# Kernel tuning notes

Hardware: AMD Instinct MI355X
Metric: run time of the kernel (lower is better)

## Reference

```python
import jax, jax.numpy as jnp
import numpy as np

# Config matching init_kwargs
D_MODEL = 1024   # input_size
D_HEAD = 2048    # head_size (expert hidden)
N_EXPERTS = 8
TOP_K = 2


def setup_inputs() -> dict:
    key = jax.random.key(0)
    k_x, k_g, k_w1, k_b1, k_w2, k_b2 = jax.random.split(key, 6)
    B, S = 4, 1024
    x = jax.random.normal(k_x, (B, S, D_MODEL), dtype=jnp.float32)
    # f_gate: nn.Linear(input_size, num_experts, bias=False) -> weight [E, D]
    gate_w = jax.random.normal(k_g, (N_EXPERTS, D_MODEL), dtype=jnp.float32) * 0.02
    # experts: ParallelExperts weights [E, in, out]
    s1 = 1.0 / D_MODEL
    s2 = 1.0 / D_HEAD
    w1 = jax.random.uniform(k_w1, (N_EXPERTS, D_MODEL, D_HEAD), jnp.float32, -s1, s1)
    b1 = jax.random.uniform(k_b1, (N_EXPERTS, D_HEAD), jnp.float32, -s1, s1)
    w2 = jax.random.uniform(k_w2, (N_EXPERTS, D_HEAD, D_MODEL), jnp.float32, -s2, s2)
    b2 = jax.random.uniform(k_b2, (N_EXPERTS, D_MODEL), jnp.float32, -s2, s2)
    return {"x": x, "gate_w": gate_w, "w1": w1, "b1": b1, "w2": w2, "b2": b2}


def reference(x, gate_w, w1, b1, w2, b2):
    B, S, D = x.shape
    xt = x.reshape(-1, D)                                   # [N, D]
    N = xt.shape[0]
    # --- gating (noisy_gating=False, eval path of top_k_gating) ---
    logits = xt @ gate_w.T                                  # [N, E]
    probs = jax.nn.softmax(logits, axis=-1)
    top_g, top_i = jax.lax.top_k(probs, TOP_K)              # [N, k]
    # gates = zeros.scatter(1, top_k_indices, top_k_gates)
    gates = jnp.zeros_like(probs).at[jnp.arange(N)[:, None], top_i].set(top_g)  # [N, E]
    # --- dispatch / grouped GEMM / combine ---
    # Equivalent dense-per-expert form: gates[n,e]==0 for non-routed tokens,
    # so y[n] = sum_e gates[n,e] * f_e(x[n]) exactly matches the
    # sort/scatter + per-expert torch.mm dispatch of ParallelLinear.
    y = jnp.zeros_like(xt)
    for e in range(N_EXPERTS):
        h = jax.nn.gelu(xt @ w1[e] + b1[e], approximate=False)  # [N, H]
        y = y + gates[:, e:e + 1] * (h @ w2[e] + b2[e])
    return y.reshape(B, S, D)
```

## Files before the change

### kernel.cpp

```cpp
#include <hip/hip_runtime.h>
#include <hip/hip_bf16.h>
#include <cstdint>
#include <cstddef>

#define N_TOK 4096
#define DM    1024
#define DH    2048
#define NE    8
#define BM    128
#define BN    128
#define BK    64
#define MAXT  80
#define HROWS (MAXT * BM)

typedef unsigned short u16t;
typedef __attribute__((ext_vector_type(4))) float          f32x4;
typedef __attribute__((ext_vector_type(8))) unsigned short u16x8;

__device__ __forceinline__ u16t f2b(float f) {
  union { float f; unsigned u; } v; v.f = f;
  return (u16t)((v.u + 0x7FFFu + ((v.u >> 16) & 1u)) >> 16);
}

__device__ __forceinline__ void gload16(const void* g, void* l) {
  auto gp = (const __attribute__((address_space(1))) unsigned int*)(uintptr_t)g;
  auto lp = (__attribute__((address_space(3))) unsigned int*)(uintptr_t)l;
  __builtin_amdgcn_global_load_lds(gp, lp, 16, 0, 0);
}

__device__ __forceinline__ void mfma16(f32x4& c, u16x8 a, u16x8 b) {
  asm("v_mfma_f32_16x16x32_bf16 %0, %1, %2, %0" : "+v"(c) : "v"(a), "v"(b));
}

__global__ void k_cvt_x(const float* __restrict__ x, u16t* __restrict__ x16) {
  int i = blockIdx.x * blockDim.x + threadIdx.x;
  float4 v = reinterpret_cast<const float4*>(x)[i];
  ushort4 o;
  o.x = f2b(v.x); o.y = f2b(v.y); o.z = f2b(v.z); o.w = f2b(v.w);
  reinterpret_cast<ushort4*>(x16)[i] = o;
}

__global__ void k_tr_cvt(const float* __restrict__ src, u16t* __restrict__ dst, int R, int C) {
  __shared__ float t[64][65];
  const float* s = src + (size_t)blockIdx.z * R * C;
  u16t* d = dst + (size_t)blockIdx.z * R * C;
  int r0 = blockIdx.y * 64, c0 = blockIdx.x * 64;
#pragma unroll
  for (int i = 0; i < 16; ++i) {
    int idx = i * 256 + threadIdx.x;
    int r = idx >> 6, c = idx & 63;
    t[r][c] = s[(size_t)(r0 + r) * C + (c0 + c)];
  }
  __syncthreads();
#pragma unroll
  for (int i = 0; i < 16; ++i) {
    int idx = i * 256 + threadIdx.x;
    int rr = idx >> 6, cc = idx & 63;
    d[(size_t)(c0 + rr) * R + (r0 + cc)] = f2b(t[cc][rr]);
  }
}

__global__ void __launch_bounds__(256) k_gate(const float* __restrict__ x,
                                              const float* __restrict__ gw,
                                              int* __restrict__ topi,
                                              float* __restrict__ topg) {
  __shared__ float gws[NE * DM];
  int tid = threadIdx.x;
#pragma unroll
  for (int i = 0; i < NE * DM / 256; ++i) gws[i * 256 + tid] = gw[i * 256 + tid];
  __syncthreads();
  int wv = tid >> 6, lane = tid & 63;
  int t = blockIdx.x * 4 + wv;
  float acc[NE];
#pragma unroll
  for (int e = 0; e < NE; ++e) acc[e] = 0.f;
  const float* xr = x + (size_t)t * DM;
#pragma unroll
  for (int c = 0; c < DM / 64; ++c) {
    float xv = xr[c * 64 + lane];
#pragma unroll
    for (int e = 0; e < NE; ++e) acc[e] += xv * gws[e * DM + c * 64 + lane];
  }
#pragma unroll
  for (int e = 0; e < NE; ++e) {
#pragma unroll
    for (int m = 1; m < 64; m <<= 1) acc[e] += __shfl_xor(acc[e], m);
  }
  float mx = acc[0];
#pragma unroll
  for (int e = 1; e < NE; ++e) mx = fmaxf(mx, acc[e]);
  float p[NE], s = 0.f;
#pragma unroll
  for (int e = 0; e < NE; ++e) { p[e] = expf(acc[e] - mx); s += p[e]; }
  float inv = 1.f / s;
#pragma unroll
  for (int e = 0; e < NE; ++e) p[e] *= inv;
  int i1 = 0; float g1 = p[0];
#pragma unroll
  for (int e = 1; e < NE; ++e) if (p[e] > g1) { g1 = p[e]; i1 = e; }
  int i2 = -1; float g2 = -1.f;
#pragma unroll
  for (int e = 0; e < NE; ++e) if (e != i1 && p[e] > g2) { g2 = p[e]; i2 = e; }
  if (lane == 0) {
    topi[t * 2 + 0] = i1; topi[t * 2 + 1] = i2;
    topg[t * 2 + 0] = g1; topg[t * 2 + 1] = g2;
  }
}

__global__ void __launch_bounds__(1024) k_scan(const int* __restrict__ topi,
                                               int* __restrict__ offe,
                                               int* __restrict__ cur64,
                                               int* __restrict__ te,
                                               int* __restrict__ trs,
                                               int* __restrict__ tnr,
                                               int* __restrict__ ntiles) {
  __shared__ int hist[NE];
  int tid = threadIdx.x;
  if (tid < NE) { hist[tid] = 0; cur64[tid * 16] = 0; }
  __syncthreads();
  int lc[NE];
#pragma unroll
  for (int e = 0; e < NE; ++e) lc[e] = 0;
#pragma unroll
  for (int i = 0; i < (N_TOK * 2) / 1024; ++i) {
    int v = topi[tid * ((N_TOK * 2) / 1024) + i];
#pragma unroll
    for (int e = 0; e < NE; ++e) lc[e] += (v == e);
  }
#pragma unroll
  for (int e = 0; e < NE; ++e) {
#pragma unroll
    for (int m = 1; m < 64; m <<= 1) lc[e] += __shfl_xor(lc[e], m);
  }
  if ((tid & 63) == 0) {
#pragma unroll
    for (int e = 0; e < NE; ++e) atomicAdd(&hist[e], lc[e]);
  }
  __syncthreads();
  if (tid == 0) {
    int off = 0, nt = 0;
    for (int e = 0; e < NE; ++e) {
      offe[e] = off;
      int c = hist[e];
      for (int i = 0; i < c; i += BM) {
        te[nt] = e; trs[nt] = off + i; tnr[nt] = min(BM, c - i); ++nt;
      }
      off += c;
    }
    *ntiles = nt;
  }
}

__global__ void k_scatter(const int* __restrict__ topi, const int* __restrict__ offe,
                          int* __restrict__ cur64, int* __restrict__ pair) {
  int t = blockIdx.x * blockDim.x + threadIdx.x;
  int lane = threadIdx.x & 63;
#pragma unroll
  for (int s = 0; s < 2; ++s) {
    int e = topi[t * 2 + s];
    int pos = 0;
#pragma unroll
    for (int ee = 0; ee < NE; ++ee) {
      unsigned long long mask = __ballot(e == ee);
      if (e == ee) {
        int rank = __popcll(mask & ((1ull << lane) - 1ull));
        int leader = __ffsll((long long)mask) - 1;
        int base = 0;
        if (lane == leader) base = atomicAdd(&cur64[ee * 16], (int)__popcll(mask));
        base = __shfl(base, leader);
        pos = offe[ee] + base + rank;
      }
    }
    pair[pos] = t * 2 + s;
  }
}

__global__ void __launch_bounds__(256, 2) k_gemm1(
    const u16t* __restrict__ x16, const u16t* __restrict__ w1t,
    const float* __restrict__ b1, u16t* __restrict__ h16,
    const int* __restrict__ pair, const int* __restrict__ te,
    const int* __restrict__ trs, const int* __restrict__ tnr,
    const int* __restrict__ ntiles) {
  int ty = blockIdx.y;
  if (ty >= *ntiles) return;
  int e = te[ty], rs = trs[ty], nr = tnr[ty];
  int n0 = blockIdx.x * BN;
  __shared__ u16t As[BM * BK];
  __shared__ u16t Bs[BN * BK];
  __shared__ int tok[BM];
  int tid = threadIdx.x;
  if (tid < BM) {
    int r = tid;
    int p = rs + (r < nr ? r : nr - 1);
    tok[r] = pair[p] >> 1;
  }
  __syncthreads();
  const u16t* aptr[4]; const u16t* bptr[4];
#pragma unroll
  for (int it = 0; it < 4; ++it) {
    int idx = it * 256 + tid;
    int r = idx >> 3, c = idx & 7;
    int cs = c ^ (r & 7);
    aptr[it] = x16 + (size_t)tok[r] * DM + cs * 8;
    bptr[it] = w1t + (size_t)e * DH * DM + (size_t)(n0 + r) * DM + cs * 8;
  }
  f32x4 acc[4][4];
#pragma unroll
  for (int m = 0; m < 4; ++m)
#pragma unroll
    for (int n = 0; n < 4; ++n) acc[m][n] = {0.f, 0.f, 0.f, 0.f};
  int lane = tid & 63, wv = tid >> 6;
  int wr = (wv >> 1) * 64, wc = (wv & 1) * 64;
  for (int k0 = 0; k0 < DM; k0 += BK) {
#pragma unroll
    for (int it = 0; it < 4; ++it) {
      int idx = it * 256 + tid;
      gload16(aptr[it] + k0, &As[idx * 8]);
      gload16(bptr[it] + k0, &Bs[idx * 8]);
    }
    __syncthreads();
#pragma unroll
    for (int kk = 0; kk < 2; ++kk) {
      u16x8 af[4], bf[4];
#pragma unroll
      for (int m = 0; m < 4; ++m) {
        int row = wr + m * 16 + (lane & 15);
        int cs = (kk * 4 + (lane >> 4)) ^ (row & 7);
        af[m] = *reinterpret_cast<const u16x8*>(&As[row * BK + cs * 8]);
      }
#pragma unroll
      for (int n = 0; n < 4; ++n) {
        int row = wc + n * 16 + (lane & 15);
        int cs = (kk * 4 + (lane >> 4)) ^ (row & 7);
        bf[n] = *reinterpret_cast<const u16x8*>(&Bs[row * BK + cs * 8]);
      }
#pragma unroll
      for (int m = 0; m < 4; ++m)
#pragma unroll
        for (int n = 0; n < 4; ++n) mfma16(acc[m][n], af[m], bf[n]);
    }
    __syncthreads();
  }
#pragma unroll
  for (int n = 0; n < 4; ++n) {
    int col = n0 + wc + n * 16 + (lane & 15);
    float bias = b1[e * DH + col];
#pragma unroll
    for (int m = 0; m < 4; ++m) {
#pragma unroll
      for (int r = 0; r < 4; ++r) {
        int rl = wr + m * 16 + ((lane >> 4) << 2) + r;
        if (rl < nr) {
          float z = acc[m][n][r] + bias;
          float g = 0.5f * z * (1.0f + erff(z * 0.70710678118654752440f));
          h16[(size_t)(rs + rl) * DH + col] = f2b(g);
        }
      }
    }
  }
}

__global__ void __launch_bounds__(256, 2) k_gemm2(
    const u16t* __restrict__ h16, const u16t* __restrict__ w2t,
    const float* __restrict__ b2, float* __restrict__ out,
    const int* __restrict__ pair, const float* __restrict__ topg,
    const int* __restrict__ te, const int* __restrict__ trs,
    const int* __restrict__ tnr, const int* __restrict__ ntiles) {
  int ty = blockIdx.y;
  if (ty >= *ntiles) return;
  int e = te[ty], rs = trs[ty], nr = tnr[ty];
  int n0 = blockIdx.x * BN;
  __shared__ u16t As[BM * BK];
  __shared__ u16t Bs[BN * BK];
  __shared__ int tsl[BM];
  __shared__ float gl[BM];
  int tid = threadIdx.x;
  if (tid < BM) {
    int r = tid;
    int p = rs + (r < nr ? r : nr - 1);
    int ts = pair[p];
    tsl[r] = ts;
    gl[r] = topg[ts];
  }
  __syncthreads();
  const u16t* aptr[4]; const u16t* bptr[4];
#pragma unroll
  for (int it = 0; it < 4; ++it) {
    int idx = it * 256 + tid;
    int r = idx >> 3, c = idx & 7;
    int cs = c ^ (r & 7);
    aptr[it] = h16 + (size_t)(rs + r) * DH + cs * 8;
    bptr[it] = w2t + (size_t)e * DM * DH + (size_t)(n0 + r) * DH + cs * 8;
  }
  f32x4 acc[4][4];
#pragma unroll
  for (int m = 0; m < 4; ++m)
#pragma unroll
    for (int n = 0; n < 4; ++n) acc[m][n] = {0.f, 0.f, 0.f, 0.f};
  int lane = tid & 63, wv = tid >> 6;
  int wr = (wv >> 1) * 64, wc = (wv & 1) * 64;
  for (int k0 = 0; k0 < DH; k0 += BK) {
#pragma unroll
    for (int it = 0; it < 4; ++it) {
      int idx = it * 256 + tid;
      gload16(aptr[it] + k0, &As[idx * 8]);
      gload16(bptr[it] + k0, &Bs[idx * 8]);
    }
    __syncthreads();
#pragma unroll
    for (int kk = 0; kk < 2; ++kk) {
      u16x8 af[4], bf[4];
#pragma unroll
      for (int m = 0; m < 4; ++m) {
        int row = wr + m * 16 + (lane & 15);
        int cs = (kk * 4 + (lane >> 4)) ^ (row & 7);
        af[m] = *reinterpret_cast<const u16x8*>(&As[row * BK + cs * 8]);
      }
#pragma unroll
      for (int n = 0; n < 4; ++n) {
        int row = wc + n * 16 + (lane & 15);
        int cs = (kk * 4 + (lane >> 4)) ^ (row & 7);
        bf[n] = *reinterpret_cast<const u16x8*>(&Bs[row * BK + cs * 8]);
      }
#pragma unroll
      for (int m = 0; m < 4; ++m)
#pragma unroll
        for (int n = 0; n < 4; ++n) mfma16(acc[m][n], af[m], bf[n]);
    }
    __syncthreads();
  }
  float bias[4];
#pragma unroll
  for (int n = 0; n < 4; ++n) bias[n] = b2[e * DM + n0 + wc + n * 16 + (lane & 15)];
#pragma unroll
  for (int m = 0; m < 4; ++m) {
#pragma unroll
    for (int r = 0; r < 4; ++r) {
      int rl = wr + m * 16 + ((lane >> 4) << 2) + r;
      if (rl < nr) {
        int ts = tsl[rl];
        float g = gl[rl];
        float* orow = out + (size_t)(ts >> 1) * DM;
#pragma unroll
        for (int n = 0; n < 4; ++n) {
          int col = n0 + wc + n * 16 + (lane & 15);
          float v = g * (acc[m][n][r] + bias[n]);
          unsafeAtomicAdd(&orow[col], v);
        }
      }
    }
  }
}

extern "C" void kernel_launch(void* const* d_in, const int* in_sizes, int n_in,
                              void* d_out, int out_size, void* d_ws, size_t ws_size,
                              hipStream_t stream) {
  const float* x  = (const float*)d_in[0];
  const float* gw = (const float*)d_in[1];
  const float* w1 = (const float*)d_in[2];
  const float* b1 = (const float*)d_in[3];
  const float* w2 = (const float*)d_in[4];
  const float* b2 = (const float*)d_in[5];
  float* out = (float*)d_out;
  char* ws = (char*)d_ws;

  size_t o = 0;
  auto alloc = [&](size_t b) { size_t p = o; o += (b + 255) & ~(size_t)255; return p; };
  size_t X16  = alloc((size_t)N_TOK * DM * 2);
  size_t W1T  = alloc((size_t)NE * DH * DM * 2);
  size_t W2T  = alloc((size_t)NE * DM * DH * 2);
  size_t HB   = alloc((size_t)HROWS * DH * 2);
  size_t TOPI = alloc((size_t)N_TOK * 2 * 4);
  size_t TOPG = alloc((size_t)N_TOK * 2 * 4);
  size_t PAIR = alloc((size_t)HROWS * 4);
  size_t CUR  = alloc(NE * 64);
  size_t OFE  = alloc(64);
  size_t TE   = alloc(MAXT * 4);
  size_t TRS  = alloc(MAXT * 4);
  size_t TNR  = alloc(MAXT * 4);
  size_t NT   = alloc(64);
  (void)ws_size; (void)in_sizes; (void)n_in;

  hipMemsetAsync(out, 0, (size_t)out_size * 4, stream);

  k_cvt_x<<<N_TOK * DM / 1024, 256, 0, stream>>>(x, (u16t*)(ws + X16));
  k_tr_cvt<<<dim3(DH / 64, DM / 64, NE), 256, 0, stream>>>(w1, (u16t*)(ws + W1T), DM, DH);
  k_tr_cvt<<<dim3(DM / 64, DH / 64, NE), 256, 0, stream>>>(w2, (u16t*)(ws + W2T), DH, DM);
  k_gate<<<N_TOK / 4, 256, 0, stream>>>(x, gw, (int*)(ws + TOPI), (float*)(ws + TOPG));
  k_scan<<<1, 1024, 0, stream>>>((int*)(ws + TOPI), (int*)(ws + OFE), (int*)(ws + CUR),
                                 (int*)(ws + TE), (int*)(ws + TRS), (int*)(ws + TNR),
                                 (int*)(ws + NT));
  k_scatter<<<N_TOK / 256, 256, 0, stream>>>((int*)(ws + TOPI), (int*)(ws + OFE),
                                             (int*)(ws + CUR), (int*)(ws + PAIR));
  k_gemm1<<<dim3(DH / BN, MAXT), 256, 0, stream>>>(
      (const u16t*)(ws + X16), (const u16t*)(ws + W1T), b1, (u16t*)(ws + HB),
      (const int*)(ws + PAIR), (const int*)(ws + TE), (const int*)(ws + TRS),
      (const int*)(ws + TNR), (const int*)(ws + NT));
  k_gemm2<<<dim3(DM / BN, MAXT), 256, 0, stream>>>(
      (const u16t*)(ws + HB), (const u16t*)(ws + W2T), b2, out,
      (const int*)(ws + PAIR), (const float*)(ws + TOPG), (const int*)(ws + TE),
      (const int*)(ws + TRS), (const int*)(ws + TNR), (const int*)(ws + NT));
}
```

Before: 221.0 us.

## Double-buffer LDS tiles in both expert GEMM kernels to overlap loads

Both grouped GEMM kernels now use two LDS buffers for the A and B tiles. The next K-slice is prefetched into the alternate buffer while MFMAs consume the current one, which hides global-load latency behind compute. The cost is double the LDS per block (about 64KB plus metadata), which may limit the two-blocks-per-CU occupancy target. The trailing synchronisation presumably still separates iterations.

```diff
diff --git a/kernel.cpp b/kernel.cpp
--- a/kernel.cpp
+++ b/kernel.cpp
@@ -185,8 +185,8 @@
   if (ty >= *ntiles) return;
   int e = te[ty], rs = trs[ty], nr = tnr[ty];
   int n0 = blockIdx.x * BN;
-  __shared__ u16t As[BM * BK];
-  __shared__ u16t Bs[BN * BK];
+  __shared__ u16t As[2][BM * BK];
+  __shared__ u16t Bs[2][BN * BK];
   __shared__ int tok[BM];
   int tid = threadIdx.x;
   if (tid < BM) {
@@ -211,14 +211,25 @@
     for (int n = 0; n < 4; ++n) acc[m][n] = {0.f, 0.f, 0.f, 0.f};
   int lane = tid & 63, wv = tid >> 6;
   int wr = (wv >> 1) * 64, wc = (wv & 1) * 64;
-  for (int k0 = 0; k0 < DM; k0 += BK) {
-#pragma unroll
-    for (int it = 0; it < 4; ++it) {
-      int idx = it * 256 + tid;
-      gload16(aptr[it] + k0, &As[idx * 8]);
-      gload16(bptr[it] + k0, &Bs[idx * 8]);
-    }
-    __syncthreads();
+#pragma unroll
+  for (int it = 0; it < 4; ++it) {
+    int idx = it * 256 + tid;
+    gload16(aptr[it], &As[0][idx * 8]);
+    gload16(bptr[it], &Bs[0][idx * 8]);
+  }
+  __syncthreads();
+  const int NK = DM / BK;
+  for (int ks = 0; ks < NK; ++ks) {
+    int cur = ks & 1;
+    if (ks + 1 < NK) {
+      int k1 = (ks + 1) * BK;
+#pragma unroll
+      for (int it = 0; it < 4; ++it) {
+        int idx = it * 256 + tid;
+        gload16(aptr[it] + k1, &As[cur ^ 1][idx * 8]);
+        gload16(bptr[it] + k1, &Bs[cur ^ 1][idx * 8]);
+      }
+    }
 #pragma unroll
     for (int kk = 0; kk < 2; ++kk) {
       u16x8 af[4], bf[4];
@@ -226,13 +237,13 @@
       for (int m = 0; m < 4; ++m) {
         int row = wr + m * 16 + (lane & 15);
         int cs = (kk * 4 + (lane >> 4)) ^ (row & 7);
-        af[m] = *reinterpret_cast<const u16x8*>(&As[row * BK + cs * 8]);
+        af[m] = *reinterpret_cast<const u16x8*>(&As[cur][row * BK + cs * 8]);
       }
 #pragma unroll
       for (int n = 0; n < 4; ++n) {
         int row = wc + n * 16 + (lane & 15);
         int cs = (kk * 4 + (lane >> 4)) ^ (row & 7);
-        bf[n] = *reinterpret_cast<const u16x8*>(&Bs[row * BK + cs * 8]);
+        bf[n] = *reinterpret_cast<const u16x8*>(&Bs[cur][row * BK + cs * 8]);
       }
 #pragma unroll
       for (int m = 0; m < 4; ++m)
@@ -270,8 +281,8 @@
   if (ty >= *ntiles) return;
   int e = te[ty], rs = trs[ty], nr = tnr[ty];
   int n0 = blockIdx.x * BN;
-  __shared__ u16t As[BM * BK];
-  __shared__ u16t Bs[BN * BK];
+  __shared__ u16t As[2][BM * BK];
+  __shared__ u16t Bs[2][BN * BK];
   __shared__ int tsl[BM];
   __shared__ float gl[BM];
   int tid = threadIdx.x;
@@ -299,14 +310,25 @@
     for (int n = 0; n < 4; ++n) acc[m][n] = {0.f, 0.f, 0.f, 0.f};
   int lane = tid & 63, wv = tid >> 6;
   int wr = (wv >> 1) * 64, wc = (wv & 1) * 64;
-  for (int k0 = 0; k0 < DH; k0 += BK) {
-#pragma unroll
-    for (int it = 0; it < 4; ++it) {
-      int idx = it * 256 + tid;
-      gload16(aptr[it] + k0, &As[idx * 8]);
-      gload16(bptr[it] + k0, &Bs[idx * 8]);
-    }
-    __syncthreads();
+#pragma unroll
+  for (int it = 0; it < 4; ++it) {
+    int idx = it * 256 + tid;
+    gload16(aptr[it], &As[0][idx * 8]);
+    gload16(bptr[it], &Bs[0][idx * 8]);
+  }
+  __syncthreads();
+  const int NK = DH / BK;
+  for (int ks = 0; ks < NK; ++ks) {
+    int cur = ks & 1;
+    if (ks + 1 < NK) {
+      int k1 = (ks + 1) * BK;
+#pragma unroll
+      for (int it = 0; it < 4; ++it) {
+        int idx = it * 256 + tid;
+        gload16(aptr[it] + k1, &As[cur ^ 1][idx * 8]);
+        gload16(bptr[it] + k1, &Bs[cur ^ 1][idx * 8]);
+      }
+    }
 #pragma unroll
     for (int kk = 0; kk < 2; ++kk) {
       u16x8 af[4], bf[4];
@@ -314,13 +336,13 @@
       for (int m = 0; m < 4; ++m) {
         int row = wr + m * 16 + (lane & 15);
         int cs = (kk * 4 + (lane >> 4)) ^ (row & 7);
-        af[m] = *reinterpret_cast<const u16x8*>(&As[row * BK + cs * 8]);
+        af[m] = *reinterpret_cast<const u16x8*>(&As[cur][row * BK + cs * 8]);
       }
 #pragma unroll
       for (int n = 0; n < 4; ++n) {
         int row = wc + n * 16 + (lane & 15);
         int cs = (kk * 4 + (lane >> 4)) ^ (row & 7);
-        bf[n] = *reinterpret_cast<const u16x8*>(&Bs[row * BK + cs * 8]);
+        bf[n] = *reinterpret_cast<const u16x8*>(&Bs[cur][row * BK + cs * 8]);
       }
 #pragma unroll
       for (int m = 0; m < 4; ++m)
```

New measurement: 245.0 us. +10.9%, slower.
